# Kernel optimization log

Hardware: AMD Instinct MI355X
Metric: run time of the kernel (lower is better)

## Reference

```python
import jax, jax.numpy as jnp
import numpy as np

B, S, D, H = 2, 2048, 1024, 16
DK = D // H

def setup_inputs() -> dict:
    key = jax.random.key(0)
    ks = jax.random.split(key, 9)
    s = 1.0 / np.sqrt(D)
    return {
        "query": jax.random.normal(ks[0], (B, S, D), dtype=jnp.float32),
        "Wq": jax.random.uniform(ks[1], (D, D), jnp.float32, -s, s),
        "bq": jax.random.uniform(ks[2], (D,), jnp.float32, -s, s),
        "Wk": jax.random.uniform(ks[3], (D, D), jnp.float32, -s, s),
        "bk": jax.random.uniform(ks[4], (D,), jnp.float32, -s, s),
        "Wv": jax.random.uniform(ks[5], (D, D), jnp.float32, -s, s),
        "bv": jax.random.uniform(ks[6], (D,), jnp.float32, -s, s),
        "Wo": jax.random.uniform(ks[7], (D, D), jnp.float32, -s, s),
        "bo": jax.random.uniform(ks[8], (D,), jnp.float32, -s, s),
    }

def reference(query, Wq, bq, Wk, bk, Wv, bv, Wo, bo):
    # q/k/v projections, reshape to [B,H,S,DK]
    def proj(x, W, b):
        return (x @ W + b).reshape(B, S, H, DK).transpose(0, 2, 1, 3)
    q = proj(query, Wq, bq)
    k = proj(query, Wk, bk)
    v = proj(query, Wv, bv)
    scores = jnp.einsum("bhqd,bhkd->bhqk", q, k) / jnp.sqrt(jnp.float32(DK))
    attn = jax.nn.softmax(scores, axis=-1)
    out = jnp.einsum("bhqk,bhkd->bhqd", attn, v)  # [B,H,S,DK]
    concat = out.transpose(0, 2, 1, 3).reshape(B, S, D)
    return concat @ Wo + bo
```

## Files before the change

kernel.cpp:

```cpp
#include <hip/hip_runtime.h>

#define S_LEN  2048
#define DMODEL 1024
#define NHEAD  16
#define DKDIM  64
#define NBATCH 2

typedef short bf16x8 __attribute__((ext_vector_type(8)));
typedef float f32x4  __attribute__((ext_vector_type(4)));

__device__ __forceinline__ unsigned short f2b(float f){
  unsigned int x = __float_as_uint(f);
  return (unsigned short)((x + 0x7FFFu + ((x >> 16) & 1u)) >> 16);
}
__device__ __forceinline__ unsigned short f2b_rhu(float f){
  return (unsigned short)((__float_as_uint(f) + 0x8000u) >> 16);
}
__device__ __forceinline__ bf16x8 ld8(const unsigned short* p){
  return *reinterpret_cast<const bf16x8*>(p);
}
__device__ __forceinline__ void gld16(const unsigned short* g, unsigned short* l){
  __builtin_amdgcn_global_load_lds(
      (const __attribute__((address_space(1))) unsigned int*)(uintptr_t)g,
      (__attribute__((address_space(3))) unsigned int*)(uintptr_t)l,
      16, 0, 0);
}

__global__ __launch_bounds__(256) void convert_x(
    const float* __restrict__ X, unsigned short* __restrict__ Xc)
{
  const size_t i0 = ((size_t)blockIdx.x * 256 + threadIdx.x) * 8;
  const float4 a = *reinterpret_cast<const float4*>(X + i0);
  const float4 b = *reinterpret_cast<const float4*>(X + i0 + 4);
  bf16x8 o;
  o[0]=(short)f2b(a.x); o[1]=(short)f2b(a.y); o[2]=(short)f2b(a.z); o[3]=(short)f2b(a.w);
  o[4]=(short)f2b(b.x); o[5]=(short)f2b(b.y); o[6]=(short)f2b(b.z); o[7]=(short)f2b(b.w);
  *reinterpret_cast<bf16x8*>(Xc + i0) = o;
}

__global__ __launch_bounds__(256) void transpose_w(
    const float* __restrict__ W0, const float* __restrict__ W1,
    const float* __restrict__ W2, const float* __restrict__ W3,
    unsigned short* __restrict__ Wt)
{
  __shared__ unsigned short tile[64][65];
  const float* src = (blockIdx.z==0)?W0:(blockIdx.z==1)?W1:(blockIdx.z==2)?W2:W3;
  unsigned short* dst = Wt + (size_t)blockIdx.z * DMODEL * DMODEL;
  const int r0 = blockIdx.x * 64, c0 = blockIdx.y * 64;
  #pragma unroll
  for(int t=0;t<16;t++){
    int idx = threadIdx.x + t*256;
    int r = idx >> 6, c = idx & 63;
    tile[r][c] = f2b(src[(size_t)(r0+r)*DMODEL + (c0+c)]);
  }
  __syncthreads();
  #pragma unroll
  for(int t=0;t<16;t++){
    int idx = threadIdx.x + t*256;
    int r = idx >> 6, c = idx & 63;
    dst[(size_t)(c0+r)*DMODEL + (r0+c)] = tile[c][r];
  }
}

__global__ __launch_bounds__(256) void gemm_qkv(
    const unsigned short* __restrict__ Xc,
    const unsigned short* __restrict__ WtBase,
    const float* __restrict__ bq,
    const float* __restrict__ bk,
    const float* __restrict__ bv,
    unsigned short* __restrict__ q_ws,
    unsigned short* __restrict__ k_ws,
    unsigned short* __restrict__ vT_ws)
{
  __shared__ __align__(16) unsigned short sA[128][32];
  __shared__ __align__(16) unsigned short sB[128][32];
  const int z = blockIdx.z;
  const unsigned short* Wt   = WtBase + (size_t)z * DMODEL * DMODEL;
  const float* bias = (z==0) ? bq : ((z==1) ? bk : bv);
  const int m0 = blockIdx.x * 128, n0 = blockIdx.y * 128;
  const int tid = threadIdx.x;
  const int w = tid >> 6, lane = tid & 63, quad = lane >> 4, lm = lane & 15;
  const int wm = (w & 1) * 64, wn = (w >> 1) * 64;
  const int srow = lane >> 2, scol = (lane & 3) * 8;

  f32x4 acc[4][4];
  #pragma unroll
  for(int i=0;i<4;i++)
    #pragma unroll
    for(int j=0;j<4;j++){ f32x4 z4 = {0.f,0.f,0.f,0.f}; acc[i][j] = z4; }

  for(int k0=0;k0<DMODEL;k0+=32){
    #pragma unroll
    for(int j=0;j<2;j++){
      gld16(Xc + (size_t)(m0 + w*32 + j*16 + srow)*DMODEL + k0 + scol, &sA[w*32 + j*16][0]);
      gld16(Wt + (size_t)(n0 + w*32 + j*16 + srow)*DMODEL + k0 + scol, &sB[w*32 + j*16][0]);
    }
    __syncthreads();
    bf16x8 a[4], b[4];
    #pragma unroll
    for(int i=0;i<4;i++) a[i] = ld8(&sA[wm + i*16 + lm][quad*8]);
    #pragma unroll
    for(int j=0;j<4;j++) b[j] = ld8(&sB[wn + j*16 + lm][quad*8]);
    #pragma unroll
    for(int i=0;i<4;i++)
      #pragma unroll
      for(int j=0;j<4;j++)
        acc[i][j] = __builtin_amdgcn_mfma_f32_16x16x32_bf16(a[i], b[j], acc[i][j], 0, 0, 0);
    __syncthreads();
  }

  #pragma unroll
  for(int j=0;j<4;j++){
    const int n  = n0 + wn + j*16 + lm;
    const float bb = bias[n];
    const int h_ = n >> 6, d_ = n & 63;
    #pragma unroll
    for(int i=0;i<4;i++){
      #pragma unroll
      for(int r=0;r<4;r++){
        const int m  = m0 + wm + i*16 + quad*4 + r;
        const int b_ = m >> 11, s_ = m & 2047;
        const unsigned short o = f2b(acc[i][j][r] + bb);
        if(z == 0)      q_ws [((size_t)(b_*NHEAD + h_)*S_LEN + s_)*DKDIM + d_] = o;
        else if(z == 1) k_ws [((size_t)(b_*NHEAD + h_)*S_LEN + s_)*DKDIM + d_] = o;
        else            vT_ws[((size_t)(b_*NHEAD + h_)*DKDIM + d_)*S_LEN + s_] = o;
      }
    }
  }
}

__global__ __launch_bounds__(256) void flash_attn(
    const unsigned short* __restrict__ q_ws,
    const unsigned short* __restrict__ k_ws,
    const unsigned short* __restrict__ vT_ws,
    unsigned short* __restrict__ attn_c)
{
  __shared__ __align__(16) unsigned short kt[2][64][72];
  __shared__ __align__(16) unsigned short vt[2][64][72];
  __shared__ __align__(16) unsigned short p_lds[4][32][72];
  const int bh = blockIdx.y;
  const int b_ = bh >> 4, h_ = bh & 15;
  const int tid = threadIdx.x;
  const int w = tid >> 6, lane = tid & 63, quad = lane >> 4, lm = lane & 15;
  const int r0 = blockIdx.x * 128 + w * 32;

  const unsigned short* qp = q_ws  + ((size_t)bh * S_LEN + r0) * DKDIM;
  const unsigned short* kp = k_ws  + (size_t)bh * S_LEN * DKDIM;
  const unsigned short* vp = vT_ws + (size_t)bh * DKDIM * S_LEN;

  bf16x8 qf[2][2];
  #pragma unroll
  for(int g=0;g<2;g++)
    #pragma unroll
    for(int c=0;c<2;c++)
      qf[g][c] = ld8(qp + (size_t)(g*16 + lm)*DKDIM + c*32 + quad*8);

  f32x4 o_acc[2][4];
  #pragma unroll
  for(int g=0;g<2;g++)
    #pragma unroll
    for(int d=0;d<4;d++){ f32x4 z4 = {0.f,0.f,0.f,0.f}; o_acc[g][d] = z4; }
  float rsum[2][4] = {{0.f,0.f,0.f,0.f},{0.f,0.f,0.f,0.f}};

  const int srow = lane >> 3;
  const int scol = (lane & 7) * 8;

  bf16x8 kreg[2], vreg[2];
  #pragma unroll
  for(int p=0;p<2;p++){
    kreg[p] = ld8(kp + (size_t)(w*16 + p*8 + srow)*DKDIM + scol);
    vreg[p] = ld8(vp + (size_t)(w*16 + p*8 + srow)*S_LEN + scol);
  }
  #pragma unroll
  for(int p=0;p<2;p++){
    *reinterpret_cast<bf16x8*>(&kt[0][w*16 + p*8 + srow][scol]) = kreg[p];
    *reinterpret_cast<bf16x8*>(&vt[0][w*16 + p*8 + srow][scol]) = vreg[p];
  }
  __syncthreads();

  for(int t=0;t<32;t++){
    const int buf = t & 1;
    if(t < 31){
      const int jn = (t+1)*64;
      #pragma unroll
      for(int p=0;p<2;p++){
        kreg[p] = ld8(kp + (size_t)(jn + w*16 + p*8 + srow)*DKDIM + scol);
        vreg[p] = ld8(vp + (size_t)(w*16 + p*8 + srow)*S_LEN + jn + scol);
      }
    }
    #pragma unroll
    for(int s=0;s<4;s++){
      bf16x8 k0 = ld8(&kt[buf][s*16 + lm][quad*8]);
      bf16x8 k1 = ld8(&kt[buf][s*16 + lm][32 + quad*8]);
      #pragma unroll
      for(int g=0;g<2;g++){
        f32x4 z4 = {0.f,0.f,0.f,0.f};
        f32x4 sc = __builtin_amdgcn_mfma_f32_16x16x32_bf16(qf[g][0], k0, z4, 0,0,0);
        sc       = __builtin_amdgcn_mfma_f32_16x16x32_bf16(qf[g][1], k1, sc, 0,0,0);
        #pragma unroll
        for(int r=0;r<4;r++){
          float e = __expf(sc[r]*0.125f);
          rsum[g][r] += e;
          p_lds[w][g*16 + quad*4 + r][s*16 + lm] = f2b_rhu(e);
        }
      }
    }
    #pragma unroll
    for(int ch=0;ch<2;ch++){
      bf16x8 pf0 = ld8(&p_lds[w][lm     ][ch*32 + quad*8]);
      bf16x8 pf1 = ld8(&p_lds[w][16 + lm][ch*32 + quad*8]);
      #pragma unroll
      for(int d=0;d<4;d++){
        bf16x8 vf = ld8(&vt[buf][d*16 + lm][ch*32 + quad*8]);
        o_acc[0][d] = __builtin_amdgcn_mfma_f32_16x16x32_bf16(pf0, vf, o_acc[0][d], 0,0,0);
        o_acc[1][d] = __builtin_amdgcn_mfma_f32_16x16x32_bf16(pf1, vf, o_acc[1][d], 0,0,0);
      }
    }
    if(t < 31){
      const int nb = 1 - buf;
      #pragma unroll
      for(int p=0;p<2;p++){
        *reinterpret_cast<bf16x8*>(&kt[nb][w*16 + p*8 + srow][scol]) = kreg[p];
        *reinterpret_cast<bf16x8*>(&vt[nb][w*16 + p*8 + srow][scol]) = vreg[p];
      }
    }
    __syncthreads();
  }

  float rinv[2][4];
  #pragma unroll
  for(int g=0;g<2;g++)
    #pragma unroll
    for(int r=0;r<4;r++){
      float s = rsum[g][r];
      s += __shfl_xor(s,1);
      s += __shfl_xor(s,2);
      s += __shfl_xor(s,4);
      s += __shfl_xor(s,8);
      rinv[g][r] = __frcp_rn(s);
    }

  #pragma unroll
  for(int g=0;g<2;g++)
    #pragma unroll
    for(int d=0;d<4;d++)
      #pragma unroll
      for(int r=0;r<4;r++){
        const int row = r0 + g*16 + quad*4 + r;
        const int col = h_*DKDIM + d*16 + lm;
        attn_c[((size_t)(b_*S_LEN + row))*DMODEL + col] = f2b(o_acc[g][d][r] * rinv[g][r]);
      }
}

__global__ __launch_bounds__(256) void gemm_out(
    const unsigned short* __restrict__ A,
    const unsigned short* __restrict__ Wt,
    const float* __restrict__ bias,
    float* __restrict__ out)
{
  __shared__ __align__(16) unsigned short sA[128][32];
  __shared__ __align__(16) unsigned short sB[128][32];
  const int m0 = blockIdx.x * 128, n0 = blockIdx.y * 128;
  const int tid = threadIdx.x;
  const int w = tid >> 6, lane = tid & 63, quad = lane >> 4, lm = lane & 15;
  const int wm = (w & 1) * 64, wn = (w >> 1) * 64;
  const int srow = lane >> 2, scol = (lane & 3) * 8;

  f32x4 acc[4][4];
  #pragma unroll
  for(int i=0;i<4;i++)
    #pragma unroll
    for(int j=0;j<4;j++){ f32x4 z4 = {0.f,0.f,0.f,0.f}; acc[i][j] = z4; }

  for(int k0=0;k0<DMODEL;k0+=32){
    #pragma unroll
    for(int j=0;j<2;j++){
      gld16(A  + (size_t)(m0 + w*32 + j*16 + srow)*DMODEL + k0 + scol, &sA[w*32 + j*16][0]);
      gld16(Wt + (size_t)(n0 + w*32 + j*16 + srow)*DMODEL + k0 + scol, &sB[w*32 + j*16][0]);
    }
    __syncthreads();
    bf16x8 a[4], b[4];
    #pragma unroll
    for(int i=0;i<4;i++) a[i] = ld8(&sA[wm + i*16 + lm][quad*8]);
    #pragma unroll
    for(int j=0;j<4;j++) b[j] = ld8(&sB[wn + j*16 + lm][quad*8]);
    #pragma unroll
    for(int i=0;i<4;i++)
      #pragma unroll
      for(int j=0;j<4;j++)
        acc[i][j] = __builtin_amdgcn_mfma_f32_16x16x32_bf16(a[i], b[j], acc[i][j], 0, 0, 0);
    __syncthreads();
  }

  #pragma unroll
  for(int j=0;j<4;j++){
    const int n = n0 + wn + j*16 + lm;
    const float bb = bias[n];
    #pragma unroll
    for(int i=0;i<4;i++){
      #pragma unroll
      for(int r=0;r<4;r++){
        const int m = m0 + wm + i*16 + quad*4 + r;
        out[(size_t)m*DMODEL + n] = acc[i][j][r] + bb;
      }
    }
  }
}

extern "C" void kernel_launch(void* const* d_in, const int* in_sizes, int n_in,
                              void* d_out, int out_size, void* d_ws, size_t ws_size,
                              hipStream_t stream)
{
  const float* X  = (const float*)d_in[0];
  const float* Wq = (const float*)d_in[1];
  const float* bq = (const float*)d_in[2];
  const float* Wk = (const float*)d_in[3];
  const float* bk = (const float*)d_in[4];
  const float* Wv = (const float*)d_in[5];
  const float* bv = (const float*)d_in[6];
  const float* Wo = (const float*)d_in[7];
  const float* bo = (const float*)d_in[8];

  unsigned short* ws = (unsigned short*)d_ws;
  const size_t WMAT = (size_t)DMODEL * DMODEL;
  const size_t QKV  = (size_t)NBATCH * NHEAD * S_LEN * DKDIM;
  unsigned short* Wt     = ws;
  unsigned short* Xc     = ws + 4*WMAT;
  unsigned short* q_ws   = Xc + QKV;
  unsigned short* k_ws   = q_ws + QKV;
  unsigned short* vT_ws  = k_ws + QKV;
  unsigned short* attn_c = Xc;
  float* out = (float*)d_out;

  convert_x  <<<dim3(2048),     256, 0, stream>>>(X, Xc);
  transpose_w<<<dim3(16,16,4),  256, 0, stream>>>(Wq, Wk, Wv, Wo, Wt);
  gemm_qkv   <<<dim3(32,8,3),   256, 0, stream>>>(Xc, Wt, bq, bk, bv, q_ws, k_ws, vT_ws);
  flash_attn <<<dim3(16,32),    256, 0, stream>>>(q_ws, k_ws, vT_ws, attn_c);
  gemm_out   <<<dim3(32,8),     256, 0, stream>>>(attn_c, Wt + 3*WMAT, bo, out);
}
```

Before: 216.1 us.

## Halve attention rows per block and stage V-transpose stores through LDS

```diff
diff --git a/kernel.cpp b/kernel.cpp
--- a/kernel.cpp
+++ b/kernel.cpp
@@ -74,6 +74,7 @@
 {
   __shared__ __align__(16) unsigned short sA[128][32];
   __shared__ __align__(16) unsigned short sB[128][32];
+  __shared__ __align__(16) unsigned short sT[64*136];
   const int z = blockIdx.z;
   const unsigned short* Wt   = WtBase + (size_t)z * DMODEL * DMODEL;
   const float* bias = (z==0) ? bq : ((z==1) ? bk : bv);
@@ -109,22 +110,53 @@
     __syncthreads();
   }
 
-  #pragma unroll
-  for(int j=0;j<4;j++){
-    const int n  = n0 + wn + j*16 + lm;
-    const float bb = bias[n];
-    const int h_ = n >> 6, d_ = n & 63;
-    #pragma unroll
-    for(int i=0;i<4;i++){
-      #pragma unroll
-      for(int r=0;r<4;r++){
-        const int m  = m0 + wm + i*16 + quad*4 + r;
-        const int b_ = m >> 11, s_ = m & 2047;
-        const unsigned short o = f2b(acc[i][j][r] + bb);
-        if(z == 0)      q_ws [((size_t)(b_*NHEAD + h_)*S_LEN + s_)*DKDIM + d_] = o;
-        else if(z == 1) k_ws [((size_t)(b_*NHEAD + h_)*S_LEN + s_)*DKDIM + d_] = o;
-        else            vT_ws[((size_t)(b_*NHEAD + h_)*DKDIM + d_)*S_LEN + s_] = o;
-      }
+  if(z != 2){
+    #pragma unroll
+    for(int j=0;j<4;j++){
+      const int n  = n0 + wn + j*16 + lm;
+      const float bb = bias[n];
+      const int h_ = n >> 6, d_ = n & 63;
+      #pragma unroll
+      for(int i=0;i<4;i++){
+        #pragma unroll
+        for(int r=0;r<4;r++){
+          const int m  = m0 + wm + i*16 + quad*4 + r;
+          const int b_ = m >> 11, s_ = m & 2047;
+          const unsigned short o = f2b(acc[i][j][r] + bb);
+          if(z == 0) q_ws[((size_t)(b_*NHEAD + h_)*S_LEN + s_)*DKDIM + d_] = o;
+          else       k_ws[((size_t)(b_*NHEAD + h_)*S_LEN + s_)*DKDIM + d_] = o;
+        }
+      }
+    }
+  } else {
+    #pragma unroll
+    for(int hf=0; hf<2; hf++){
+      if((w >> 1) == hf){
+        #pragma unroll
+        for(int j=0;j<4;j++){
+          const int nl = j*16 + lm;
+          const float bb = bias[n0 + hf*64 + nl];
+          #pragma unroll
+          for(int i=0;i<4;i++)
+            #pragma unroll
+            for(int r=0;r<4;r++)
+              sT[nl*136 + wm + i*16 + quad*4 + r] = f2b(acc[i][j][r] + bb);
+        }
+      }
+      __syncthreads();
+      {
+        const int nl = tid >> 2, seg = tid & 3;
+        const int n  = n0 + hf*64 + nl;
+        const int h_ = n >> 6, d_ = n & 63;
+        const int b_ = m0 >> 11;
+        const int s0 = (m0 & 2047) + seg*32;
+        unsigned short* dst = vT_ws + ((size_t)(b_*NHEAD + h_)*DKDIM + d_)*S_LEN + s0;
+        #pragma unroll
+        for(int k=0;k<4;k++)
+          *reinterpret_cast<bf16x8*>(dst + k*8) =
+              *reinterpret_cast<const bf16x8*>(&sT[nl*136 + seg*32 + k*8]);
+      }
+      __syncthreads();
     }
   }
 }
@@ -137,30 +169,24 @@
 {
   __shared__ __align__(16) unsigned short kt[2][64][72];
   __shared__ __align__(16) unsigned short vt[2][64][72];
-  __shared__ __align__(16) unsigned short p_lds[4][32][72];
+  __shared__ __align__(16) unsigned short ph[4][16][40];
   const int bh = blockIdx.y;
   const int b_ = bh >> 4, h_ = bh & 15;
   const int tid = threadIdx.x;
   const int w = tid >> 6, lane = tid & 63, quad = lane >> 4, lm = lane & 15;
-  const int r0 = blockIdx.x * 128 + w * 32;
+  const int r0 = blockIdx.x * 64 + w * 16;
 
   const unsigned short* qp = q_ws  + ((size_t)bh * S_LEN + r0) * DKDIM;
   const unsigned short* kp = k_ws  + (size_t)bh * S_LEN * DKDIM;
   const unsigned short* vp = vT_ws + (size_t)bh * DKDIM * S_LEN;
 
-  bf16x8 qf[2][2];
-  #pragma unroll
-  for(int g=0;g<2;g++)
-    #pragma unroll
-    for(int c=0;c<2;c++)
-      qf[g][c] = ld8(qp + (size_t)(g*16 + lm)*DKDIM + c*32 + quad*8);
-
-  f32x4 o_acc[2][4];
-  #pragma unroll
-  for(int g=0;g<2;g++)
-    #pragma unroll
-    for(int d=0;d<4;d++){ f32x4 z4 = {0.f,0.f,0.f,0.f}; o_acc[g][d] = z4; }
-  float rsum[2][4] = {{0.f,0.f,0.f,0.f},{0.f,0.f,0.f,0.f}};
+  bf16x8 qf0 = ld8(qp + (size_t)lm*DKDIM + quad*8);
+  bf16x8 qf1 = ld8(qp + (size_t)lm*DKDIM + 32 + quad*8);
+
+  f32x4 o_acc[4];
+  #pragma unroll
+  for(int d=0;d<4;d++){ f32x4 z4 = {0.f,0.f,0.f,0.f}; o_acc[d] = z4; }
+  float rsum[4] = {0.f,0.f,0.f,0.f};
 
   const int srow = lane >> 3;
   const int scol = (lane & 7) * 8;
@@ -189,31 +215,27 @@
       }
     }
     #pragma unroll
-    for(int s=0;s<4;s++){
-      bf16x8 k0 = ld8(&kt[buf][s*16 + lm][quad*8]);
-      bf16x8 k1 = ld8(&kt[buf][s*16 + lm][32 + quad*8]);
-      #pragma unroll
-      for(int g=0;g<2;g++){
+    for(int sh=0;sh<2;sh++){
+      #pragma unroll
+      for(int s2=0;s2<2;s2++){
+        const int s = sh*2 + s2;
+        bf16x8 k0 = ld8(&kt[buf][s*16 + lm][quad*8]);
+        bf16x8 k1 = ld8(&kt[buf][s*16 + lm][32 + quad*8]);
         f32x4 z4 = {0.f,0.f,0.f,0.f};
-        f32x4 sc = __builtin_amdgcn_mfma_f32_16x16x32_bf16(qf[g][0], k0, z4, 0,0,0);
-        sc       = __builtin_amdgcn_mfma_f32_16x16x32_bf16(qf[g][1], k1, sc, 0,0,0);
+        f32x4 sc = __builtin_amdgcn_mfma_f32_16x16x32_bf16(qf0, k0, z4, 0,0,0);
+        sc       = __builtin_amdgcn_mfma_f32_16x16x32_bf16(qf1, k1, sc, 0,0,0);
         #pragma unroll
         for(int r=0;r<4;r++){
           float e = __expf(sc[r]*0.125f);
-          rsum[g][r] += e;
-          p_lds[w][g*16 + quad*4 + r][s*16 + lm] = f2b_rhu(e);
+          rsum[r] += e;
+          ph[w][quad*4 + r][s2*16 + lm] = f2b_rhu(e);
         }
       }
-    }
-    #pragma unroll
-    for(int ch=0;ch<2;ch++){
-      bf16x8 pf0 = ld8(&p_lds[w][lm     ][ch*32 + quad*8]);
-      bf16x8 pf1 = ld8(&p_lds[w][16 + lm][ch*32 + quad*8]);
+      bf16x8 pf = ld8(&ph[w][lm][quad*8]);
       #pragma unroll
       for(int d=0;d<4;d++){
-        bf16x8 vf = ld8(&vt[buf][d*16 + lm][ch*32 + quad*8]);
-        o_acc[0][d] = __builtin_amdgcn_mfma_f32_16x16x32_bf16(pf0, vf, o_acc[0][d], 0,0,0);
-        o_acc[1][d] = __builtin_amdgcn_mfma_f32_16x16x32_bf16(pf1, vf, o_acc[1][d], 0,0,0);
+        bf16x8 vf = ld8(&vt[buf][d*16 + lm][sh*32 + quad*8]);
+        o_acc[d] = __builtin_amdgcn_mfma_f32_16x16x32_bf16(pf, vf, o_acc[d], 0,0,0);
       }
     }
     if(t < 31){
@@ -227,29 +249,25 @@
     __syncthreads();
   }
 
-  float rinv[2][4];
-  #pragma unroll
-  for(int g=0;g<2;g++)
+  float rinv[4];
+  #pragma unroll
+  for(int r=0;r<4;r++){
+    float s = rsum[r];
+    s += __shfl_xor(s,1);
+    s += __shfl_xor(s,2);
+    s += __shfl_xor(s,4);
+    s += __shfl_xor(s,8);
+    rinv[r] = __frcp_rn(s);
+  }
+
+  #pragma unroll
+  for(int d=0;d<4;d++)
     #pragma unroll
     for(int r=0;r<4;r++){
-      float s = rsum[g][r];
-      s += __shfl_xor(s,1);
-      s += __shfl_xor(s,2);
-      s += __shfl_xor(s,4);
-      s += __shfl_xor(s,8);
-      rinv[g][r] = __frcp_rn(s);
-    }
-
-  #pragma unroll
-  for(int g=0;g<2;g++)
-    #pragma unroll
-    for(int d=0;d<4;d++)
-      #pragma unroll
-      for(int r=0;r<4;r++){
-        const int row = r0 + g*16 + quad*4 + r;
-        const int col = h_*DKDIM + d*16 + lm;
-        attn_c[((size_t)(b_*S_LEN + row))*DMODEL + col] = f2b(o_acc[g][d][r] * rinv[g][r]);
-      }
+      const int row = r0 + quad*4 + r;
+      const int col = h_*DKDIM + d*16 + lm;
+      attn_c[((size_t)(b_*S_LEN + row))*DMODEL + col] = f2b(o_acc[d][r] * rinv[r]);
+    }
 }
 
 __global__ __launch_bounds__(256) void gemm_out(
@@ -335,6 +353,6 @@
   convert_x  <<<dim3(2048),     256, 0, stream>>>(X, Xc);
   transpose_w<<<dim3(16,16,4),  256, 0, stream>>>(Wq, Wk, Wv, Wo, Wt);
   gemm_qkv   <<<dim3(32,8,3),   256, 0, stream>>>(Xc, Wt, bq, bk, bv, q_ws, k_ws, vT_ws);
-  flash_attn <<<dim3(16,32),    256, 0, stream>>>(q_ws, k_ws, vT_ws, attn_c);
+  flash_attn <<<dim3(32,32),    256, 0, stream>>>(q_ws, k_ws, vT_ws, attn_c);
   gemm_out   <<<dim3(32,8),     256, 0, stream>>>(attn_c, Wt + 3*WMAT, bo, out);
 }
```

Measured after the change: 228.2 us. 1.06x slower.

## Split attention keys across waves with LDS reduction and fold scale into Wq

Applied to the files above, without the earlier changes.

```diff
diff --git a/kernel.cpp b/kernel.cpp
--- a/kernel.cpp
+++ b/kernel.cpp
@@ -5,6 +5,7 @@
 #define NHEAD  16
 #define DKDIM  64
 #define NBATCH 2
+#define SCALE_Q 0.1803368801f
 
 typedef short bf16x8 __attribute__((ext_vector_type(8)));
 typedef float f32x4  __attribute__((ext_vector_type(4)));
@@ -45,13 +46,14 @@
 {
   __shared__ unsigned short tile[64][65];
   const float* src = (blockIdx.z==0)?W0:(blockIdx.z==1)?W1:(blockIdx.z==2)?W2:W3;
+  const float sc = (blockIdx.z==0) ? SCALE_Q : 1.0f;
   unsigned short* dst = Wt + (size_t)blockIdx.z * DMODEL * DMODEL;
   const int r0 = blockIdx.x * 64, c0 = blockIdx.y * 64;
   #pragma unroll
   for(int t=0;t<16;t++){
     int idx = threadIdx.x + t*256;
     int r = idx >> 6, c = idx & 63;
-    tile[r][c] = f2b(src[(size_t)(r0+r)*DMODEL + (c0+c)]);
+    tile[r][c] = f2b(src[(size_t)(r0+r)*DMODEL + (c0+c)] * sc);
   }
   __syncthreads();
   #pragma unroll
@@ -77,6 +79,7 @@
   const int z = blockIdx.z;
   const unsigned short* Wt   = WtBase + (size_t)z * DMODEL * DMODEL;
   const float* bias = (z==0) ? bq : ((z==1) ? bk : bv);
+  const float bscale = (z==0) ? SCALE_Q : 1.0f;
   const int m0 = blockIdx.x * 128, n0 = blockIdx.y * 128;
   const int tid = threadIdx.x;
   const int w = tid >> 6, lane = tid & 63, quad = lane >> 4, lm = lane & 15;
@@ -112,7 +115,7 @@
   #pragma unroll
   for(int j=0;j<4;j++){
     const int n  = n0 + wn + j*16 + lm;
-    const float bb = bias[n];
+    const float bb = bias[n] * bscale;
     const int h_ = n >> 6, d_ = n & 63;
     #pragma unroll
     for(int i=0;i<4;i++){
@@ -129,107 +132,97 @@
   }
 }
 
-__global__ __launch_bounds__(256) void flash_attn(
+__global__ __launch_bounds__(256, 2) void flash_attn(
     const unsigned short* __restrict__ q_ws,
     const unsigned short* __restrict__ k_ws,
     const unsigned short* __restrict__ vT_ws,
     unsigned short* __restrict__ attn_c)
 {
-  __shared__ __align__(16) unsigned short kt[2][64][72];
-  __shared__ __align__(16) unsigned short vt[2][64][72];
-  __shared__ __align__(16) unsigned short p_lds[4][32][72];
+  __shared__ __align__(16) unsigned short ph[4][64][40];
+  __shared__ __align__(16) float red[64][68];
+  __shared__ float rs[4][64];
   const int bh = blockIdx.y;
   const int b_ = bh >> 4, h_ = bh & 15;
   const int tid = threadIdx.x;
   const int w = tid >> 6, lane = tid & 63, quad = lane >> 4, lm = lane & 15;
-  const int r0 = blockIdx.x * 128 + w * 32;
-
-  const unsigned short* qp = q_ws  + ((size_t)bh * S_LEN + r0) * DKDIM;
-  const unsigned short* kp = k_ws  + (size_t)bh * S_LEN * DKDIM;
-  const unsigned short* vp = vT_ws + (size_t)bh * DKDIM * S_LEN;
-
-  bf16x8 qf[2][2];
-  #pragma unroll
-  for(int g=0;g<2;g++)
+  const int q0 = blockIdx.x * 64;
+
+  const unsigned short* qp = q_ws  + ((size_t)bh * S_LEN + q0) * DKDIM;
+  const unsigned short* kp = k_ws  + ((size_t)bh * S_LEN + w*32 + lm) * DKDIM + quad*8;
+  const unsigned short* vp = vT_ws + (size_t)bh * DKDIM * S_LEN + w*32 + quad*8;
+
+  bf16x8 qf[4][2];
+  #pragma unroll
+  for(int g=0;g<4;g++)
     #pragma unroll
     for(int c=0;c<2;c++)
       qf[g][c] = ld8(qp + (size_t)(g*16 + lm)*DKDIM + c*32 + quad*8);
 
-  f32x4 o_acc[2][4];
-  #pragma unroll
-  for(int g=0;g<2;g++)
+  f32x4 o_acc[4][4];
+  #pragma unroll
+  for(int g=0;g<4;g++)
     #pragma unroll
     for(int d=0;d<4;d++){ f32x4 z4 = {0.f,0.f,0.f,0.f}; o_acc[g][d] = z4; }
-  float rsum[2][4] = {{0.f,0.f,0.f,0.f},{0.f,0.f,0.f,0.f}};
-
-  const int srow = lane >> 3;
-  const int scol = (lane & 7) * 8;
-
-  bf16x8 kreg[2], vreg[2];
-  #pragma unroll
-  for(int p=0;p<2;p++){
-    kreg[p] = ld8(kp + (size_t)(w*16 + p*8 + srow)*DKDIM + scol);
-    vreg[p] = ld8(vp + (size_t)(w*16 + p*8 + srow)*S_LEN + scol);
-  }
-  #pragma unroll
-  for(int p=0;p<2;p++){
-    *reinterpret_cast<bf16x8*>(&kt[0][w*16 + p*8 + srow][scol]) = kreg[p];
-    *reinterpret_cast<bf16x8*>(&vt[0][w*16 + p*8 + srow][scol]) = vreg[p];
-  }
-  __syncthreads();
-
-  for(int t=0;t<32;t++){
-    const int buf = t & 1;
-    if(t < 31){
-      const int jn = (t+1)*64;
-      #pragma unroll
-      for(int p=0;p<2;p++){
-        kreg[p] = ld8(kp + (size_t)(jn + w*16 + p*8 + srow)*DKDIM + scol);
-        vreg[p] = ld8(vp + (size_t)(w*16 + p*8 + srow)*S_LEN + jn + scol);
-      }
-    }
-    #pragma unroll
-    for(int s=0;s<4;s++){
-      bf16x8 k0 = ld8(&kt[buf][s*16 + lm][quad*8]);
-      bf16x8 k1 = ld8(&kt[buf][s*16 + lm][32 + quad*8]);
-      #pragma unroll
-      for(int g=0;g<2;g++){
+  float rsum[4][4];
+  #pragma unroll
+  for(int g=0;g<4;g++)
+    #pragma unroll
+    for(int r=0;r<4;r++) rsum[g][r] = 0.f;
+
+  bf16x8 kc[2][2], vc[4], kn[2][2], vn[4];
+  #pragma unroll
+  for(int cg=0;cg<2;cg++)
+    #pragma unroll
+    for(int c=0;c<2;c++)
+      kc[cg][c] = ld8(kp + (size_t)(cg*16)*DKDIM + c*32);
+  #pragma unroll
+  for(int dg=0;dg<4;dg++)
+    vc[dg] = ld8(vp + (size_t)(dg*16 + lm)*S_LEN);
+
+  for(int t=0;t<16;t++){
+    if(t < 15){
+      const size_t jo = (size_t)(t+1)*128;
+      #pragma unroll
+      for(int cg=0;cg<2;cg++)
+        #pragma unroll
+        for(int c=0;c<2;c++)
+          kn[cg][c] = ld8(kp + (jo + cg*16)*DKDIM + c*32);
+      #pragma unroll
+      for(int dg=0;dg<4;dg++)
+        vn[dg] = ld8(vp + (size_t)(dg*16 + lm)*S_LEN + jo);
+    }
+    #pragma unroll
+    for(int g=0;g<4;g++){
+      #pragma unroll
+      for(int cg=0;cg<2;cg++){
         f32x4 z4 = {0.f,0.f,0.f,0.f};
-        f32x4 sc = __builtin_amdgcn_mfma_f32_16x16x32_bf16(qf[g][0], k0, z4, 0,0,0);
-        sc       = __builtin_amdgcn_mfma_f32_16x16x32_bf16(qf[g][1], k1, sc, 0,0,0);
+        f32x4 sc = __builtin_amdgcn_mfma_f32_16x16x32_bf16(qf[g][0], kc[cg][0], z4, 0,0,0);
+        sc       = __builtin_amdgcn_mfma_f32_16x16x32_bf16(qf[g][1], kc[cg][1], sc, 0,0,0);
         #pragma unroll
         for(int r=0;r<4;r++){
-          float e = __expf(sc[r]*0.125f);
+          float e = exp2f(sc[r]);
           rsum[g][r] += e;
-          p_lds[w][g*16 + quad*4 + r][s*16 + lm] = f2b_rhu(e);
+          ph[w][g*16 + quad*4 + r][cg*16 + lm] = f2b_rhu(e);
         }
       }
-    }
-    #pragma unroll
-    for(int ch=0;ch<2;ch++){
-      bf16x8 pf0 = ld8(&p_lds[w][lm     ][ch*32 + quad*8]);
-      bf16x8 pf1 = ld8(&p_lds[w][16 + lm][ch*32 + quad*8]);
-      #pragma unroll
-      for(int d=0;d<4;d++){
-        bf16x8 vf = ld8(&vt[buf][d*16 + lm][ch*32 + quad*8]);
-        o_acc[0][d] = __builtin_amdgcn_mfma_f32_16x16x32_bf16(pf0, vf, o_acc[0][d], 0,0,0);
-        o_acc[1][d] = __builtin_amdgcn_mfma_f32_16x16x32_bf16(pf1, vf, o_acc[1][d], 0,0,0);
-      }
-    }
-    if(t < 31){
-      const int nb = 1 - buf;
-      #pragma unroll
-      for(int p=0;p<2;p++){
-        *reinterpret_cast<bf16x8*>(&kt[nb][w*16 + p*8 + srow][scol]) = kreg[p];
-        *reinterpret_cast<bf16x8*>(&vt[nb][w*16 + p*8 + srow][scol]) = vreg[p];
-      }
-    }
-    __syncthreads();
-  }
-
-  float rinv[2][4];
-  #pragma unroll
-  for(int g=0;g<2;g++)
+      bf16x8 pf = ld8(&ph[w][g*16 + lm][quad*8]);
+      #pragma unroll
+      for(int dg=0;dg<4;dg++)
+        o_acc[g][dg] = __builtin_amdgcn_mfma_f32_16x16x32_bf16(pf, vc[dg], o_acc[g][dg], 0,0,0);
+    }
+    if(t < 15){
+      #pragma unroll
+      for(int cg=0;cg<2;cg++)
+        #pragma unroll
+        for(int c=0;c<2;c++) kc[cg][c] = kn[cg][c];
+      #pragma unroll
+      for(int dg=0;dg<4;dg++) vc[dg] = vn[dg];
+    }
+  }
+
+  float sred[4][4];
+  #pragma unroll
+  for(int g=0;g<4;g++)
     #pragma unroll
     for(int r=0;r<4;r++){
       float s = rsum[g][r];
@@ -237,19 +230,52 @@
       s += __shfl_xor(s,2);
       s += __shfl_xor(s,4);
       s += __shfl_xor(s,8);
-      rinv[g][r] = __frcp_rn(s);
-    }
-
-  #pragma unroll
-  for(int g=0;g<2;g++)
-    #pragma unroll
-    for(int d=0;d<4;d++)
-      #pragma unroll
-      for(int r=0;r<4;r++){
-        const int row = r0 + g*16 + quad*4 + r;
-        const int col = h_*DKDIM + d*16 + lm;
-        attn_c[((size_t)(b_*S_LEN + row))*DMODEL + col] = f2b(o_acc[g][d][r] * rinv[g][r]);
-      }
+      sred[g][r] = s;
+    }
+
+  if(w == 0){
+    #pragma unroll
+    for(int g=0;g<4;g++)
+      #pragma unroll
+      for(int dg=0;dg<4;dg++)
+        #pragma unroll
+        for(int r=0;r<4;r++)
+          red[g*16 + quad*4 + r][dg*16 + lm] = o_acc[g][dg][r];
+  }
+  if(lm == 0){
+    #pragma unroll
+    for(int g=0;g<4;g++)
+      #pragma unroll
+      for(int r=0;r<4;r++)
+        rs[w][g*16 + quad*4 + r] = sred[g][r];
+  }
+  __syncthreads();
+  if(w != 0){
+    #pragma unroll
+    for(int g=0;g<4;g++)
+      #pragma unroll
+      for(int dg=0;dg<4;dg++)
+        #pragma unroll
+        for(int r=0;r<4;r++)
+          atomicAdd(&red[g*16 + quad*4 + r][dg*16 + lm], o_acc[g][dg][r]);
+  }
+  __syncthreads();
+
+  {
+    const int rl = lane >> 2, cs = (lane & 3) * 16;
+    const int row = w*16 + rl;
+    const float s = rs[0][row] + rs[1][row] + rs[2][row] + rs[3][row];
+    const float ri = __frcp_rn(s);
+    bf16x8 o1, o2;
+    #pragma unroll
+    for(int k=0;k<8;k++){
+      o1[k] = (short)f2b(red[row][cs + k] * ri);
+      o2[k] = (short)f2b(red[row][cs + 8 + k] * ri);
+    }
+    unsigned short* op = attn_c + ((size_t)(b_*S_LEN + q0 + row))*DMODEL + h_*DKDIM + cs;
+    *reinterpret_cast<bf16x8*>(op)     = o1;
+    *reinterpret_cast<bf16x8*>(op + 8) = o2;
+  }
 }
 
 __global__ __launch_bounds__(256) void gemm_out(
@@ -335,6 +361,6 @@
   convert_x  <<<dim3(2048),     256, 0, stream>>>(X, Xc);
   transpose_w<<<dim3(16,16,4),  256, 0, stream>>>(Wq, Wk, Wv, Wo, Wt);
   gemm_qkv   <<<dim3(32,8,3),   256, 0, stream>>>(Xc, Wt, bq, bk, bv, q_ws, k_ws, vT_ws);
-  flash_attn <<<dim3(16,32),    256, 0, stream>>>(q_ws, k_ws, vT_ws, attn_c);
+  flash_attn <<<dim3(32,32),    256, 0, stream>>>(q_ws, k_ws, vT_ws, attn_c);
   gemm_out   <<<dim3(32,8),     256, 0, stream>>>(attn_c, Wt + 3*WMAT, bo, out);
 }
```

After: 279.1 us. 29.2% more time.
